# Performance work log

Hardware: AMD Instinct MI355X
Metric: run time of the kernel (lower is better)

Reference implementation:

```python
import jax, jax.numpy as jnp
import numpy as np

E, H, I, B, K = 8, 2048, 5632, 1024, 2


def setup_inputs() -> dict:
    key = jax.random.key(0)
    k_x, k_id, k_w, k_g, k_u, k_d = jax.random.split(key, 6)
    x = jax.random.normal(k_x, (B, H), dtype=jnp.float32)
    expert_ids = jax.random.randint(k_id, (B, K), 0, E).astype(jnp.int32)
    ew = jax.random.uniform(k_w, (B, K), dtype=jnp.float32)
    expert_weights = ew / jnp.sum(ew, axis=-1, keepdims=True)  # router probs, sum to 1
    scale = 0.02
    gate_weights = jax.random.normal(k_g, (E, H, I), dtype=jnp.float32) * scale
    up_weights = jax.random.normal(k_u, (E, H, I), dtype=jnp.float32) * scale
    down_weights = jax.random.normal(k_d, (E, I, H), dtype=jnp.float32) * scale
    return {
        "x": x,
        "expert_ids": expert_ids,
        "expert_weights": expert_weights,
        "gate_weights": gate_weights,
        "up_weights": up_weights,
        "down_weights": down_weights,
    }


def reference(x, expert_ids, expert_weights, gate_weights, up_weights, down_weights):
    # Faithful math: per token t, expert e = expert_ids[t,k]:
    #   out[t] = sum_k expert_weights[t,k] * (silu(x W_gate_e) * (x W_up_e)) W_down_e
    # Implemented as dense all-expert GEMMs + select, which computes the
    # identical per-expert matmuls as the original's gathered-weight einsums
    # without materializing the [B,K,H,I] gathered weight tensor.
    gate_all = jnp.einsum('bh,ehi->bei', x, gate_weights)        # [B,E,I]
    up_all = jnp.einsum('bh,ehi->bei', x, up_weights)            # [B,E,I]
    act_all = jax.nn.silu(gate_all) * up_all                     # [B,E,I]
    out_all = jnp.einsum('bei,eih->beh', act_all, down_weights)  # [B,E,H]
    # Select the top_k experts' outputs per token: [B,K,H]
    sel = jnp.take_along_axis(out_all, expert_ids[:, :, None], axis=1)
    return jnp.sum(sel * expert_weights[:, :, None], axis=1)     # [B,H]
```

## Files before the change

kernel.cpp:

```cpp
#include <hip/hip_runtime.h>
#include <hip/hip_bf16.h>

#define E_ 8
#define H_ 2048
#define I_ 5632
#define B_ 1024
#define K_ 2
#define NROWS (B_*K_)

#define BM 128
#define MAXT 24

#define GBN 128
#define GBK 32
#define NK2 (H_/GBK)
#define NYG2 (I_/GBN)

#define BN 64
#define BK 64
#define NKD (I_/BK)
#define NYD (H_/BN)

typedef __attribute__((ext_vector_type(8))) __bf16 bf16x8;
typedef __attribute__((ext_vector_type(4))) float f32x4;

union BF4 { __bf16 b[4]; uint2 q; };
union BF8 { __bf16 b[8]; uint4 q; };

__device__ __forceinline__ void gld_lds16(const void* g, void* l) {
  __builtin_amdgcn_global_load_lds(
      (const __attribute__((address_space(1))) void*)g,
      (__attribute__((address_space(3))) void*)l, 16, 0, 0);
}

#define GLOAD4(dst, ptr) asm volatile("global_load_dwordx4 %0, %1, off" : "=v"(dst) : "v"(ptr))
#define WAITV(N) do { asm volatile("s_waitcnt vmcnt(" #N ")" ::: "memory"); __builtin_amdgcn_sched_barrier(0); } while(0)
#define WAITL()  do { asm volatile("s_waitcnt lgkmcnt(0)" ::: "memory"); __builtin_amdgcn_sched_barrier(0); } while(0)
#define BAR()    __builtin_amdgcn_s_barrier()

#define MSK(c) (((c)&7) ^ (((c)>>2)&7))

__global__ void cvtx_kernel(const float* __restrict__ x, __bf16* __restrict__ xb) {
  int i = (blockIdx.x * 256 + threadIdx.x) * 8;
  float4 a = *(const float4*)(x + i);
  float4 b = *(const float4*)(x + i + 4);
  BF8 r;
  r.b[0] = (__bf16)a.x; r.b[1] = (__bf16)a.y; r.b[2] = (__bf16)a.z; r.b[3] = (__bf16)a.w;
  r.b[4] = (__bf16)b.x; r.b[5] = (__bf16)b.y; r.b[6] = (__bf16)b.z; r.b[7] = (__bf16)b.w;
  *(uint4*)(xb + i) = r.q;
}

__global__ void route_kernel(const int* __restrict__ ids,
                             int* __restrict__ counts, int* __restrict__ offsets,
                             int* __restrict__ tlist, int* __restrict__ row_of,
                             int* __restrict__ tile_e, int* __restrict__ tile_m) {
  __shared__ int sc[E_], sp[E_], so[E_];
  int t = threadIdx.x;
  if (t < E_) { sc[t] = 0; sp[t] = 0; }
  __syncthreads();
  for (int idx = t; idx < NROWS; idx += 256) atomicAdd(&sc[ids[idx]], 1);
  __syncthreads();
  if (t == 0) {
    int acc = 0;
    for (int e = 0; e < E_; ++e) { so[e] = acc; acc += sc[e]; }
    int nt = 0;
    for (int e = 0; e < E_; ++e)
      for (int m0 = 0; m0 < sc[e]; m0 += BM) { tile_e[nt] = e; tile_m[nt] = m0; ++nt; }
    for (; nt < MAXT; ++nt) { tile_e[nt] = 0; tile_m[nt] = 0x7FFFFFFF; }
  }
  __syncthreads();
  for (int idx = t; idx < NROWS; idx += 256) {
    int e = ids[idx];
    int slot = atomicAdd(&sp[e], 1);
    int row = so[e] + slot;
    tlist[row] = idx / K_;
    row_of[idx] = row;
  }
  if (t < E_) { counts[t] = sc[t]; offsets[t] = so[t]; }
}

__global__ __launch_bounds__(256, 2) void gateup_kernel(
    const __bf16* __restrict__ xb, const float* __restrict__ gw,
    const float* __restrict__ uw, const int* __restrict__ counts,
    const int* __restrict__ offsets, const int* __restrict__ tlist,
    const int* __restrict__ tile_e, const int* __restrict__ tile_m,
    __bf16* __restrict__ act)
{
  extern __shared__ char smem[];
  char* As0 = smem;
  char* As1 = smem + 8192;
  char* Bg0 = smem + 16384;
  char* Bu0 = smem + 24576;
  char* Bg1 = smem + 32768;
  char* Bu1 = smem + 40960;

  const int id = blockIdx.x;
  const int w  = (id & 7) * 132 + (id >> 3);
  const int tt = w % MAXT;
  const int ny = w / MAXT;
  const int e  = tile_e[tt];
  const int m0 = tile_m[tt];
  const int cnt = counts[e];
  if (m0 >= cnt) return;
  const int off = offsets[e];
  const int n0 = ny * GBN;

  const int tid  = threadIdx.x;
  const int lane = tid & 63;
  const int wave = tid >> 6;
  const int wr = (wave >> 1) * 64;
  const int wc = (wave & 1) * 64;

  const __bf16* asrc0; const __bf16* asrc1;
  int ad0, ad1;
  {
    const __bf16* s[2]; int d[2];
#pragma unroll
    for (int j = 0; j < 2; ++j) {
      int g = j*256 + tid;
      int ks = g >> 7;
      int sl = g & 127;
      int r  = sl ^ (ks << 2);
      int rr = m0 + r; if (rr >= cnt) rr = cnt - 1;
      int tok = tlist[off + rr];
      s[j] = xb + (size_t)tok * H_ + ks*8;
      d[j] = g * 16;
    }
    asrc0=s[0]; asrc1=s[1]; ad0=d[0]; ad1=d[1];
  }

  const int q  = tid & 31;
  const int kb = (tid >> 5) * 4;
  const float* pg0 = gw + ((size_t)e*H_ + kb + 0)*I_ + n0 + 4*q;
  const float* pg1 = gw + ((size_t)e*H_ + kb + 1)*I_ + n0 + 4*q;
  const float* pg2 = gw + ((size_t)e*H_ + kb + 2)*I_ + n0 + 4*q;
  const float* pg3 = gw + ((size_t)e*H_ + kb + 3)*I_ + n0 + 4*q;
  const float* pu0 = uw + ((size_t)e*H_ + kb + 0)*I_ + n0 + 4*q;
  const float* pu1 = uw + ((size_t)e*H_ + kb + 1)*I_ + n0 + 4*q;
  const float* pu2 = uw + ((size_t)e*H_ + kb + 2)*I_ + n0 + 4*q;
  const float* pu3 = uw + ((size_t)e*H_ + kb + 3)*I_ + n0 + 4*q;
  int bw0, bw1, bw2, bw3;
  {
    int ksw  = kb >> 3;
    int half = (kb & 4) << 1;
    int b[4];
#pragma unroll
    for (int i = 0; i < 4; ++i) {
      int slot = (q ^ (i << 2)) + (i << 5);
      b[i] = ksw*2048 + slot*16 + half;
    }
    bw0=b[0]; bw1=b[1]; bw2=b[2]; bw3=b[3];
  }

  const int ks = lane >> 4;
  int aofs0;
  int bofs0, bofs1, bofs2, bofs3;
  {
    int r0 = wr + (lane & 15);
    aofs0 = ks*2048 + ((r0 ^ (ks << 2)) << 4);
    int c0 = wc + (lane & 15);
    int ii = c0 & 3;
    int bb[4];
#pragma unroll
    for (int ni = 0; ni < 4; ++ni) {
      int qq = (c0 >> 2) + ni*4;
      int slot = (qq ^ (ii << 2)) + (ii << 5);
      bb[ni] = ks*2048 + slot*16;
    }
    bofs0=bb[0]; bofs1=bb[1]; bofs2=bb[2]; bofs3=bb[3];
  }

  f32x4 vg_0,vg_1,vg_2,vg_3, vu_0,vu_1,vu_2,vu_3;

  f32x4 accg[4][4], accu[4][4];
#pragma unroll
  for (int i = 0; i < 4; ++i)
#pragma unroll
    for (int j = 0; j < 4; ++j) {
      accg[i][j] = (f32x4){0.f,0.f,0.f,0.f};
      accu[i][j] = (f32x4){0.f,0.f,0.f,0.f};
    }

  auto COMPUTE = [&](const char* Ap, const char* Bgp, const char* Bup) {
    __builtin_amdgcn_s_setprio(1);
    bf16x8 a0 = *(const bf16x8*)(Ap + aofs0 + 0*256);
    bf16x8 a1 = *(const bf16x8*)(Ap + aofs0 + 1*256);
    bf16x8 a2 = *(const bf16x8*)(Ap + aofs0 + 2*256);
    bf16x8 a3 = *(const bf16x8*)(Ap + aofs0 + 3*256);
#define MM(ACC, A, B) ACC = __builtin_amdgcn_mfma_f32_16x16x32_bf16(A, B, ACC, 0,0,0)
    {
      bf16x8 b0 = *(const bf16x8*)(Bgp + bofs0);
      bf16x8 b1 = *(const bf16x8*)(Bgp + bofs1);
      bf16x8 b2 = *(const bf16x8*)(Bgp + bofs2);
      bf16x8 b3 = *(const bf16x8*)(Bgp + bofs3);
      MM(accg[0][0], a0, b0); MM(accg[1][0], a1, b0); MM(accg[2][0], a2, b0); MM(accg[3][0], a3, b0);
      MM(accg[0][1], a0, b1); MM(accg[1][1], a1, b1); MM(accg[2][1], a2, b1); MM(accg[3][1], a3, b1);
      MM(accg[0][2], a0, b2); MM(accg[1][2], a1, b2); MM(accg[2][2], a2, b2); MM(accg[3][2], a3, b2);
      MM(accg[0][3], a0, b3); MM(accg[1][3], a1, b3); MM(accg[2][3], a2, b3); MM(accg[3][3], a3, b3);
    }
    {
      bf16x8 b0 = *(const bf16x8*)(Bup + bofs0);
      bf16x8 b1 = *(const bf16x8*)(Bup + bofs1);
      bf16x8 b2 = *(const bf16x8*)(Bup + bofs2);
      bf16x8 b3 = *(const bf16x8*)(Bup + bofs3);
      MM(accu[0][0], a0, b0); MM(accu[1][0], a1, b0); MM(accu[2][0], a2, b0); MM(accu[3][0], a3, b0);
      MM(accu[0][1], a0, b1); MM(accu[1][1], a1, b1); MM(accu[2][1], a2, b1); MM(accu[3][1], a3, b1);
      MM(accu[0][2], a0, b2); MM(accu[1][2], a1, b2); MM(accu[2][2], a2, b2); MM(accu[3][2], a3, b2);
      MM(accu[0][3], a0, b3); MM(accu[1][3], a1, b3); MM(accu[2][3], a2, b3); MM(accu[3][3], a3, b3);
    }
#undef MM
    __builtin_amdgcn_s_setprio(0);
  };

#define GU_PF(KPF) do { size_t o_ = (size_t)(KPF)*(size_t)GBK*(size_t)I_; \
    GLOAD4(vg_0, pg0+o_); GLOAD4(vu_0, pu0+o_); \
    GLOAD4(vg_1, pg1+o_); GLOAD4(vu_1, pu1+o_); \
    GLOAD4(vg_2, pg2+o_); GLOAD4(vu_2, pu2+o_); \
    GLOAD4(vg_3, pg3+o_); GLOAD4(vu_3, pu3+o_); } while(0)

#define GU_CVW1(BB, V0, V1, V2, V3, BWI, I) do { BF4 p_; \
    p_.b[0]=(__bf16)V0[I]; p_.b[1]=(__bf16)V1[I]; p_.b[2]=(__bf16)V2[I]; p_.b[3]=(__bf16)V3[I]; \
    *(uint2*)((BB)+BWI) = p_.q; } while(0)

#define GU_CVW(BG, BU) do { \
    GU_CVW1(BG, vg_0, vg_1, vg_2, vg_3, bw0, 0); \
    GU_CVW1(BG, vg_0, vg_1, vg_2, vg_3, bw1, 1); \
    GU_CVW1(BG, vg_0, vg_1, vg_2, vg_3, bw2, 2); \
    GU_CVW1(BG, vg_0, vg_1, vg_2, vg_3, bw3, 3); \
    GU_CVW1(BU, vu_0, vu_1, vu_2, vu_3, bw0, 0); \
    GU_CVW1(BU, vu_0, vu_1, vu_2, vu_3, bw1, 1); \
    GU_CVW1(BU, vu_0, vu_1, vu_2, vu_3, bw2, 2); \
    GU_CVW1(BU, vu_0, vu_1, vu_2, vu_3, bw3, 3); } while(0)

#define GU_GLDA(DST, KPF) do { size_t k_ = (size_t)(KPF)*(size_t)GBK; \
    gld_lds16(asrc0 + k_, (DST)+ad0); gld_lds16(asrc1 + k_, (DST)+ad1); } while(0)

  GU_PF(0);
  WAITV(0);
  GU_CVW(Bg0, Bu0);
  GU_GLDA(As0, 0);
  GU_PF(1);
  WAITV(8);
  GU_GLDA(As1, 1);
  WAITL();
  BAR();

#pragma unroll 1
  for (int kt = 0; kt < NK2; kt += 2) {
    {
      int kpf = kt + 2; if (kpf > NK2-1) kpf = NK2-1;
      COMPUTE(As0, Bg0, Bu0);
      WAITV(1);
      GU_CVW(Bg1, Bu1);
      GU_PF(kpf);
      WAITV(8);
      WAITL();
      BAR();
      GU_GLDA(As0, kpf);
    }
    {
      int kpf = kt + 3; if (kpf > NK2-1) kpf = NK2-1;
      COMPUTE(As1, Bg1, Bu1);
      WAITV(1);
      GU_CVW(Bg0, Bu0);
      GU_PF(kpf);
      WAITV(8);
      WAITL();
      BAR();
      GU_GLDA(As1, kpf);
    }
  }
  WAITV(0);
  WAITL();

  const int rsub = (lane >> 4) * 4;
  const int csub = lane & 15;
#pragma unroll
  for (int mi = 0; mi < 4; ++mi)
#pragma unroll
    for (int j = 0; j < 4; ++j) {
      int rl = wr + mi*16 + rsub + j;
      if (m0 + rl < cnt) {
        size_t orow = (size_t)(off + m0 + rl) * I_ + n0 + wc + csub;
#pragma unroll
        for (int ni = 0; ni < 4; ++ni) {
          float g = accg[mi][ni][j];
          float u = accu[mi][ni][j];
          float sg = g / (1.0f + __expf(-g));
          act[orow + ni*16] = (__bf16)(sg * u);
        }
      }
    }
#undef GU_PF
#undef GU_CVW
#undef GU_CVW1
#undef GU_GLDA
}

__global__ __launch_bounds__(256, 3) void down_kernel(
    const __bf16* __restrict__ act, const float* __restrict__ dw,
    const int* __restrict__ counts, const int* __restrict__ offsets,
    const int* __restrict__ tile_e, const int* __restrict__ tile_m,
    float* __restrict__ rowbuf)
{
  extern __shared__ char smem[];
  char* As0 = smem;
  char* As1 = smem + 16384;
  char* Bs0 = smem + 32768;
  char* Bs1 = smem + 40960;

  const int id = blockIdx.x;
  const int w  = (id & 7) * 96 + (id >> 3);
  const int tt = w % MAXT;
  const int ny = w / MAXT;
  const int e  = tile_e[tt];
  const int m0 = tile_m[tt];
  const int cnt = counts[e];
  if (m0 >= cnt) return;
  const int off = offsets[e];
  const int n0 = ny * BN;

  const int tid  = threadIdx.x;
  const int lane = tid & 63;
  const int wave = tid >> 6;
  const int wr = (wave >> 1) * 64;
  const int wc = (wave & 1) * 32;

  const __bf16* asrc0; const __bf16* asrc1; const __bf16* asrc2; const __bf16* asrc3;
  int ad0, ad1, ad2, ad3;
  {
    const __bf16* s[4]; int d[4];
#pragma unroll
    for (int i = 0; i < 4; ++i) {
      int f = i*256 + tid;
      int r = f >> 3, cs = f & 7;
      int rr = m0 + r; if (rr >= cnt) rr = cnt - 1;
      s[i] = act + (size_t)(off + rr) * I_ + ((cs ^ (r & 7)) << 3);
      d[i] = f * 16;
    }
    asrc0=s[0]; asrc1=s[1]; asrc2=s[2]; asrc3=s[3];
    ad0=d[0]; ad1=d[1]; ad2=d[2]; ad3=d[3];
  }

  const int cq = tid & 15;
  const int kb = (tid >> 4) * 4;
  const float* pd0 = dw + ((size_t)e*I_ + kb + 0)*H_ + n0 + 4*cq;
  const float* pd1 = dw + ((size_t)e*I_ + kb + 1)*H_ + n0 + 4*cq;
  const float* pd2 = dw + ((size_t)e*I_ + kb + 2)*H_ + n0 + 4*cq;
  const float* pd3 = dw + ((size_t)e*I_ + kb + 3)*H_ + n0 + 4*cq;
  const int slot = kb >> 3;
  const int half = (kb & 4) << 1;
  int bw0, bw1, bw2, bw3;
  {
    int b[4];
#pragma unroll
    for (int i = 0; i < 4; ++i) {
      int c = 4*cq + i;
      b[i] = c*128 + ((slot ^ MSK(c)) << 4) + half;
    }
    bw0=b[0]; bw1=b[1]; bw2=b[2]; bw3=b[3];
  }

  f32x4 vdA_0,vdA_1,vdA_2,vdA_3;
  f32x4 vdB_0,vdB_1,vdB_2,vdB_3;

  f32x4 acc[4][2];
#pragma unroll
  for (int i = 0; i < 4; ++i)
#pragma unroll
    for (int j = 0; j < 2; ++j) acc[i][j] = (f32x4){0.f,0.f,0.f,0.f};

  auto COMPUTE = [&](const char* Ab, const char* Bb) {
    __builtin_amdgcn_s_setprio(1);
#pragma unroll
    for (int kk = 0; kk < 2; ++kk) {
      const int ks = kk*4 + (lane >> 4);
      const int r0 = wr + (lane & 15);
      const int swa = (ks ^ (r0 & 7)) << 4;
      bf16x8 a0 = *(const bf16x8*)(Ab + (r0 +  0)*128 + swa);
      bf16x8 a1 = *(const bf16x8*)(Ab + (r0 + 16)*128 + swa);
      bf16x8 a2 = *(const bf16x8*)(Ab + (r0 + 32)*128 + swa);
      bf16x8 a3 = *(const bf16x8*)(Ab + (r0 + 48)*128 + swa);
      const int c0 = wc + (lane & 15);
      const int swb0 = (ks ^ MSK(c0)) << 4;
      const int swb1 = swb0 ^ (4 << 4);
      bf16x8 b0 = *(const bf16x8*)(Bb + c0*128 + swb0);
      bf16x8 b1 = *(const bf16x8*)(Bb + (c0+16)*128 + swb1);
      acc[0][0] = __builtin_amdgcn_mfma_f32_16x16x32_bf16(a0, b0, acc[0][0], 0,0,0);
      acc[1][0] = __builtin_amdgcn_mfma_f32_16x16x32_bf16(a1, b0, acc[1][0], 0,0,0);
      acc[2][0] = __builtin_amdgcn_mfma_f32_16x16x32_bf16(a2, b0, acc[2][0], 0,0,0);
      acc[3][0] = __builtin_amdgcn_mfma_f32_16x16x32_bf16(a3, b0, acc[3][0], 0,0,0);
      acc[0][1] = __builtin_amdgcn_mfma_f32_16x16x32_bf16(a0, b1, acc[0][1], 0,0,0);
      acc[1][1] = __builtin_amdgcn_mfma_f32_16x16x32_bf16(a1, b1, acc[1][1], 0,0,0);
      acc[2][1] = __builtin_amdgcn_mfma_f32_16x16x32_bf16(a2, b1, acc[2][1], 0,0,0);
      acc[3][1] = __builtin_amdgcn_mfma_f32_16x16x32_bf16(a3, b1, acc[3][1], 0,0,0);
    }
    __builtin_amdgcn_s_setprio(0);
  };

#define DN_PF(S, KPF) do { size_t o_ = (size_t)(KPF)*(size_t)BK*(size_t)H_; \
    GLOAD4(vd##S##_0, pd0+o_); GLOAD4(vd##S##_1, pd1+o_); \
    GLOAD4(vd##S##_2, pd2+o_); GLOAD4(vd##S##_3, pd3+o_); } while(0)

#define DN_CVW1(BB, V0, V1, V2, V3, BWI, I) do { BF4 p_; \
    p_.b[0]=(__bf16)V0[I]; p_.b[1]=(__bf16)V1[I]; p_.b[2]=(__bf16)V2[I]; p_.b[3]=(__bf16)V3[I]; \
    *(uint2*)((BB)+BWI) = p_.q; } while(0)

#define DN_CVW(S, BB) do { \
    DN_CVW1(BB, vd##S##_0, vd##S##_1, vd##S##_2, vd##S##_3, bw0, 0); \
    DN_CVW1(BB, vd##S##_0, vd##S##_1, vd##S##_2, vd##S##_3, bw1, 1); \
    DN_CVW1(BB, vd##S##_0, vd##S##_1, vd##S##_2, vd##S##_3, bw2, 2); \
    DN_CVW1(BB, vd##S##_0, vd##S##_1, vd##S##_2, vd##S##_3, bw3, 3); } while(0)

#define DN_GLDA(DST, KPF) do { size_t k_ = (size_t)(KPF)*(size_t)BK; \
    gld_lds16(asrc0 + k_, (DST)+ad0); gld_lds16(asrc1 + k_, (DST)+ad1); \
    gld_lds16(asrc2 + k_, (DST)+ad2); gld_lds16(asrc3 + k_, (DST)+ad3); } while(0)

  DN_PF(A, 0);
  DN_GLDA(As0, 0);
  WAITV(4);
  DN_CVW(A, Bs0);
  DN_PF(B, 1);
  DN_GLDA(As1, 1);
  WAITV(8);
  WAITL();
  BAR();

#pragma unroll 1
  for (int kt = 0; kt < NKD; kt += 2) {
    {
      int kpf = kt + 2; if (kpf > NKD-1) kpf = NKD-1;
      DN_PF(A, kpf);
      COMPUTE(As0, Bs0);
      WAITV(8);
      DN_CVW(B, Bs1);
      WAITV(4);
      WAITL();
      BAR();
      DN_GLDA(As0, kpf);
    }
    {
      int kpf = kt + 3; if (kpf > NKD-1) kpf = NKD-1;
      DN_PF(B, kpf);
      COMPUTE(As1, Bs1);
      WAITV(8);
      DN_CVW(A, Bs0);
      WAITV(4);
      WAITL();
      BAR();
      DN_GLDA(As1, kpf);
    }
  }
  WAITV(0);
  WAITL();

  const int rsub = (lane >> 4) * 4;
  const int csub = lane & 15;
#pragma unroll
  for (int mi = 0; mi < 4; ++mi)
#pragma unroll
    for (int j = 0; j < 4; ++j) {
      int rl = wr + mi*16 + rsub + j;
      if (m0 + rl < cnt) {
        size_t orow = (size_t)(off + m0 + rl) * H_ + n0 + wc + csub;
#pragma unroll
        for (int cg = 0; cg < 2; ++cg)
          rowbuf[orow + cg*16] = acc[mi][cg][j];
      }
    }
#undef DN_PF
#undef DN_CVW
#undef DN_CVW1
#undef DN_GLDA
}

__global__ void combine_kernel(const float* __restrict__ ew, const int* __restrict__ row_of,
                               const float* __restrict__ rowbuf, float* __restrict__ out) {
  int idx = blockIdx.x * 256 + threadIdx.x;
  int t  = idx >> 9;
  int h4 = idx & 511;
  float w0 = ew[t*2+0], w1 = ew[t*2+1];
  int r0 = row_of[t*2+0], r1 = row_of[t*2+1];
  float4 a = *(const float4*)(rowbuf + (size_t)r0*H_ + h4*4);
  float4 b = *(const float4*)(rowbuf + (size_t)r1*H_ + h4*4);
  float4 o;
  o.x = w0*a.x + w1*b.x; o.y = w0*a.y + w1*b.y;
  o.z = w0*a.z + w1*b.z; o.w = w0*a.w + w1*b.w;
  *(float4*)(out + (size_t)idx*4) = o;
}

extern "C" void kernel_launch(void* const* d_in, const int* in_sizes, int n_in,
                              void* d_out, int out_size, void* d_ws, size_t ws_size,
                              hipStream_t stream) {
  const float* x   = (const float*)d_in[0];
  const int*   ids = (const int*)d_in[1];
  const float* ew  = (const float*)d_in[2];
  const float* gw  = (const float*)d_in[3];
  const float* uw  = (const float*)d_in[4];
  const float* dwn = (const float*)d_in[5];
  float* out = (float*)d_out;

  char* ws = (char*)d_ws;
  int* counts  = (int*)ws;
  int* offsets = counts + 8;
  int* tlist   = offsets + 8;
  int* row_of  = tlist + NROWS;
  int* tile_e  = row_of + NROWS;
  int* tile_m  = tile_e + MAXT;
  __bf16* xb   = (__bf16*)(ws + 32768);
  __bf16* act  = (__bf16*)(ws + 32768 + (size_t)B_*H_*2);
  float* rowbuf = (float*)(ws + 32768 + (size_t)B_*H_*2 + (size_t)NROWS*I_*2);

  hipFuncSetAttribute(reinterpret_cast<const void*>(&gateup_kernel),
                      hipFuncAttributeMaxDynamicSharedMemorySize, 49152);
  hipFuncSetAttribute(reinterpret_cast<const void*>(&down_kernel),
                      hipFuncAttributeMaxDynamicSharedMemorySize, 49152);

  cvtx_kernel<<<B_*H_/(256*8), 256, 0, stream>>>(x, xb);
  route_kernel<<<1, 256, 0, stream>>>(ids, counts, offsets, tlist, row_of, tile_e, tile_m);

  gateup_kernel<<<MAXT*NYG2, 256, 49152, stream>>>(xb, gw, uw, counts, offsets, tlist,
                                                   tile_e, tile_m, act);

  down_kernel<<<MAXT*NYD, 256, 49152, stream>>>(act, dwn, counts, offsets,
                                                tile_e, tile_m, rowbuf);

  combine_kernel<<<(B_*H_/4)/256, 256, 0, stream>>>(ew, row_of, rowbuf, out);
}
```

Baseline: 438.0 us.

## Switch gate/up GEMM to 32x32x16 MFMA with new LDS swizzle layout

Replaces the 16x16x32 bf16 MFMA tiling in the gate/up kernel with 32x32x16 MFMA, using 2x2 f32x16 accumulators per wave for each of gate and up. The LDS layout for A and B changes to a row-major 64-byte-per-row form with an XOR swizzle, and the fragment reads and epilogue indexing are updated to match. The prologue is also reordered so the A global-to-LDS loads are issued earlier, and the vmcnt wait counts are adjusted. The aim is fewer LDS fragment reads per MFMA and higher MFMA throughput. The cost is a riskier swizzle that could cause bank conflicts, and the waitcnt values must stay correct.

```diff
diff --git a/kernel.cpp b/kernel.cpp
--- a/kernel.cpp
+++ b/kernel.cpp
@@ -23,6 +23,7 @@
 
 typedef __attribute__((ext_vector_type(8))) __bf16 bf16x8;
 typedef __attribute__((ext_vector_type(4))) float f32x4;
+typedef __attribute__((ext_vector_type(16))) float f32x16;
 
 union BF4 { __bf16 b[4]; uint2 q; };
 union BF8 { __bf16 b[8]; uint4 q; };
@@ -117,14 +118,14 @@
     const __bf16* s[2]; int d[2];
 #pragma unroll
     for (int j = 0; j < 2; ++j) {
-      int g = j*256 + tid;
-      int ks = g >> 7;
-      int sl = g & 127;
-      int r  = sl ^ (ks << 2);
+      int f = j*256 + tid;
+      int r = f >> 2;
+      int sl = f & 3;
+      int cs = sl ^ ((r >> 1) & 3);
       int rr = m0 + r; if (rr >= cnt) rr = cnt - 1;
       int tok = tlist[off + rr];
-      s[j] = xb + (size_t)tok * H_ + ks*8;
-      d[j] = g * 16;
+      s[j] = xb + (size_t)tok * H_ + cs*8;
+      d[j] = f * 16;
     }
     asrc0=s[0]; asrc1=s[1]; ad0=d[0]; ad1=d[1];
   }
@@ -141,74 +142,62 @@
   const float* pu3 = uw + ((size_t)e*H_ + kb + 3)*I_ + n0 + 4*q;
   int bw0, bw1, bw2, bw3;
   {
-    int ksw  = kb >> 3;
+    int g    = kb >> 3;
     int half = (kb & 4) << 1;
     int b[4];
 #pragma unroll
     for (int i = 0; i < 4; ++i) {
-      int slot = (q ^ (i << 2)) + (i << 5);
-      b[i] = ksw*2048 + slot*16 + half;
+      int c = 4*q + i;
+      int slot = g ^ ((c >> 1) & 3) ^ ((c >> 5) & 3);
+      b[i] = c*64 + slot*16 + half;
     }
     bw0=b[0]; bw1=b[1]; bw2=b[2]; bw3=b[3];
   }
 
-  const int ks = lane >> 4;
-  int aofs0;
-  int bofs0, bofs1, bofs2, bofs3;
+  int aof0, aof1;
+  int bof0, bof1;
+  const int ls2 = lane >> 5;
   {
-    int r0 = wr + (lane & 15);
-    aofs0 = ks*2048 + ((r0 ^ (ks << 2)) << 4);
-    int c0 = wc + (lane & 15);
-    int ii = c0 & 3;
-    int bb[4];
-#pragma unroll
-    for (int ni = 0; ni < 4; ++ni) {
-      int qq = (c0 >> 2) + ni*4;
-      int slot = (qq ^ (ii << 2)) + (ii << 5);
-      bb[ni] = ks*2048 + slot*16;
-    }
-    bofs0=bb[0]; bofs1=bb[1]; bofs2=bb[2]; bofs3=bb[3];
+    int r0 = wr + (lane & 31);
+    int r1 = r0 + 32;
+    aof0 = r0*64 + (((r0 >> 1) & 3) << 4);
+    aof1 = r1*64 + (((r1 >> 1) & 3) << 4);
+    int c0 = wc + (lane & 31);
+    int c1 = c0 + 32;
+    bof0 = c0*64 + ((((c0 >> 1) & 3) ^ ((c0 >> 5) & 3)) << 4);
+    bof1 = c1*64 + ((((c1 >> 1) & 3) ^ ((c1 >> 5) & 3)) << 4);
   }
 
   f32x4 vg_0,vg_1,vg_2,vg_3, vu_0,vu_1,vu_2,vu_3;
 
-  f32x4 accg[4][4], accu[4][4];
-#pragma unroll
-  for (int i = 0; i < 4; ++i)
-#pragma unroll
-    for (int j = 0; j < 4; ++j) {
-      accg[i][j] = (f32x4){0.f,0.f,0.f,0.f};
-      accu[i][j] = (f32x4){0.f,0.f,0.f,0.f};
-    }
+  f32x16 accg00, accg01, accg10, accg11;
+  f32x16 accu00, accu01, accu10, accu11;
+#pragma unroll
+  for (int i = 0; i < 16; ++i) {
+    accg00[i]=0.f; accg01[i]=0.f; accg10[i]=0.f; accg11[i]=0.f;
+    accu00[i]=0.f; accu01[i]=0.f; accu10[i]=0.f; accu11[i]=0.f;
+  }
 
   auto COMPUTE = [&](const char* Ap, const char* Bgp, const char* Bup) {
     __builtin_amdgcn_s_setprio(1);
-    bf16x8 a0 = *(const bf16x8*)(Ap + aofs0 + 0*256);
-    bf16x8 a1 = *(const bf16x8*)(Ap + aofs0 + 1*256);
-    bf16x8 a2 = *(const bf16x8*)(Ap + aofs0 + 2*256);
-    bf16x8 a3 = *(const bf16x8*)(Ap + aofs0 + 3*256);
-#define MM(ACC, A, B) ACC = __builtin_amdgcn_mfma_f32_16x16x32_bf16(A, B, ACC, 0,0,0)
-    {
-      bf16x8 b0 = *(const bf16x8*)(Bgp + bofs0);
-      bf16x8 b1 = *(const bf16x8*)(Bgp + bofs1);
-      bf16x8 b2 = *(const bf16x8*)(Bgp + bofs2);
-      bf16x8 b3 = *(const bf16x8*)(Bgp + bofs3);
-      MM(accg[0][0], a0, b0); MM(accg[1][0], a1, b0); MM(accg[2][0], a2, b0); MM(accg[3][0], a3, b0);
-      MM(accg[0][1], a0, b1); MM(accg[1][1], a1, b1); MM(accg[2][1], a2, b1); MM(accg[3][1], a3, b1);
-      MM(accg[0][2], a0, b2); MM(accg[1][2], a1, b2); MM(accg[2][2], a2, b2); MM(accg[3][2], a3, b2);
-      MM(accg[0][3], a0, b3); MM(accg[1][3], a1, b3); MM(accg[2][3], a2, b3); MM(accg[3][3], a3, b3);
-    }
-    {
-      bf16x8 b0 = *(const bf16x8*)(Bup + bofs0);
-      bf16x8 b1 = *(const bf16x8*)(Bup + bofs1);
-      bf16x8 b2 = *(const bf16x8*)(Bup + bofs2);
-      bf16x8 b3 = *(const bf16x8*)(Bup + bofs3);
-      MM(accu[0][0], a0, b0); MM(accu[1][0], a1, b0); MM(accu[2][0], a2, b0); MM(accu[3][0], a3, b0);
-      MM(accu[0][1], a0, b1); MM(accu[1][1], a1, b1); MM(accu[2][1], a2, b1); MM(accu[3][1], a3, b1);
-      MM(accu[0][2], a0, b2); MM(accu[1][2], a1, b2); MM(accu[2][2], a2, b2); MM(accu[3][2], a3, b2);
-      MM(accu[0][3], a0, b3); MM(accu[1][3], a1, b3); MM(accu[2][3], a2, b3); MM(accu[3][3], a3, b3);
-    }
-#undef MM
+#pragma unroll
+    for (int kstep = 0; kstep < 2; ++kstep) {
+      const int gx = (kstep*2 + ls2) << 4;
+      bf16x8 a0 = *(const bf16x8*)(Ap + (aof0 ^ gx));
+      bf16x8 a1 = *(const bf16x8*)(Ap + (aof1 ^ gx));
+      bf16x8 g0 = *(const bf16x8*)(Bgp + (bof0 ^ gx));
+      bf16x8 g1 = *(const bf16x8*)(Bgp + (bof1 ^ gx));
+      bf16x8 u0 = *(const bf16x8*)(Bup + (bof0 ^ gx));
+      bf16x8 u1 = *(const bf16x8*)(Bup + (bof1 ^ gx));
+      accg00 = __builtin_amdgcn_mfma_f32_32x32x16_bf16(a0, g0, accg00, 0,0,0);
+      accg10 = __builtin_amdgcn_mfma_f32_32x32x16_bf16(a1, g0, accg10, 0,0,0);
+      accg01 = __builtin_amdgcn_mfma_f32_32x32x16_bf16(a0, g1, accg01, 0,0,0);
+      accg11 = __builtin_amdgcn_mfma_f32_32x32x16_bf16(a1, g1, accg11, 0,0,0);
+      accu00 = __builtin_amdgcn_mfma_f32_32x32x16_bf16(a0, u0, accu00, 0,0,0);
+      accu10 = __builtin_amdgcn_mfma_f32_32x32x16_bf16(a1, u0, accu10, 0,0,0);
+      accu01 = __builtin_amdgcn_mfma_f32_32x32x16_bf16(a0, u1, accu01, 0,0,0);
+      accu11 = __builtin_amdgcn_mfma_f32_32x32x16_bf16(a1, u1, accu11, 0,0,0);
+    }
     __builtin_amdgcn_s_setprio(0);
   };
 
@@ -236,12 +225,12 @@
     gld_lds16(asrc0 + k_, (DST)+ad0); gld_lds16(asrc1 + k_, (DST)+ad1); } while(0)
 
   GU_PF(0);
-  WAITV(0);
+  GU_GLDA(As0, 0);
+  WAITV(2);
   GU_CVW(Bg0, Bu0);
-  GU_GLDA(As0, 0);
   GU_PF(1);
-  WAITV(8);
   GU_GLDA(As1, 1);
+  WAITV(10);
   WAITL();
   BAR();
 
@@ -250,7 +239,7 @@
     {
       int kpf = kt + 2; if (kpf > NK2-1) kpf = NK2-1;
       COMPUTE(As0, Bg0, Bu0);
-      WAITV(1);
+      WAITV(2);
       GU_CVW(Bg1, Bu1);
       GU_PF(kpf);
       WAITV(8);
@@ -261,7 +250,7 @@
     {
       int kpf = kt + 3; if (kpf > NK2-1) kpf = NK2-1;
       COMPUTE(As1, Bg1, Bu1);
-      WAITV(1);
+      WAITV(2);
       GU_CVW(Bg0, Bu0);
       GU_PF(kpf);
       WAITV(8);
@@ -273,24 +262,25 @@
   WAITV(0);
   WAITL();
 
-  const int rsub = (lane >> 4) * 4;
-  const int csub = lane & 15;
-#pragma unroll
-  for (int mi = 0; mi < 4; ++mi)
-#pragma unroll
-    for (int j = 0; j < 4; ++j) {
-      int rl = wr + mi*16 + rsub + j;
-      if (m0 + rl < cnt) {
-        size_t orow = (size_t)(off + m0 + rl) * I_ + n0 + wc + csub;
-#pragma unroll
-        for (int ni = 0; ni < 4; ++ni) {
-          float g = accg[mi][ni][j];
-          float u = accu[mi][ni][j];
-          float sg = g / (1.0f + __expf(-g));
-          act[orow + ni*16] = (__bf16)(sg * u);
-        }
-      }
-    }
+  const int cl = lane & 31;
+  const int rbase = 4 * (lane >> 5);
+#define GU_EPI(ACCG, ACCU, MI, NI) do { \
+    _Pragma("unroll") \
+    for (int reg = 0; reg < 16; ++reg) { \
+      int rl = wr + (MI)*32 + (reg & 3) + 8*(reg >> 2) + rbase; \
+      if (m0 + rl < cnt) { \
+        size_t o = (size_t)(off + m0 + rl) * I_ + n0 + wc + (NI)*32 + cl; \
+        float g_ = ACCG[reg]; \
+        float u_ = ACCU[reg]; \
+        float sg_ = g_ / (1.0f + __expf(-g_)); \
+        act[o] = (__bf16)(sg_ * u_); \
+      } \
+    } } while(0)
+  GU_EPI(accg00, accu00, 0, 0);
+  GU_EPI(accg01, accu01, 0, 1);
+  GU_EPI(accg10, accu10, 1, 0);
+  GU_EPI(accg11, accu11, 1, 1);
+#undef GU_EPI
 #undef GU_PF
 #undef GU_CVW
 #undef GU_CVW1
```

Measured after the change: 433.5 us. No clear change (-1.0%).
